# Kernel tuning notes

Hardware: AMD Instinct MI355X
Metric: run time of the kernel (lower is better)

Reference implementation:

```python
import jax, jax.numpy as jnp
import numpy as np

B, H, N, D, S = 32, 4, 8192, 64, 3
EPS = 1e-10


def setup_inputs() -> dict:
    key = jax.random.key(0)
    ks = jax.random.split(key, 9)
    dev = 1.0 / np.sqrt(D + N)  # init scale from initialize_memory()
    memory = jax.random.uniform(ks[0], (B, N, D), minval=-dev, maxval=dev, dtype=jnp.float32)
    k = jax.random.normal(ks[1], (B, H, D), dtype=jnp.float32)
    beta = jax.random.uniform(ks[2], (B, H), dtype=jnp.float32) * 5.0          # key strength >= 0
    pw = jax.nn.softmax(jax.random.normal(ks[3], (B, H, N), dtype=jnp.float32), axis=-1)  # prev weights: simplex
    g = jax.random.uniform(ks[4], (B, H), dtype=jnp.float32)                    # gate in [0,1]
    s = jax.nn.softmax(jax.random.normal(ks[5], (B, H, S), dtype=jnp.float32), axis=-1)   # shift distribution
    gamma = 1.0 + 2.0 * jax.random.uniform(ks[6], (B, H), dtype=jnp.float32)    # sharpening >= 1
    erase = jax.random.uniform(ks[7], (B, H, D), dtype=jnp.float32)             # erase in [0,1]
    add = jax.random.normal(ks[8], (B, H, D), dtype=jnp.float32)
    return {"memory": memory, "k": k, "beta": beta, "pw": pw, "g": g,
            "s": s, "gamma": gamma, "erase": erase, "add": add}


def _ntm_step(memory, k, beta, pw, g, s, gamma, erase, add):
    # --- content addressing: softmax over slots of beta * cosine similarity ---
    kn = k / (jnp.linalg.norm(k, axis=-1, keepdims=True) + EPS)         # [B,H,D]
    mn = memory / (jnp.linalg.norm(memory, axis=-1, keepdims=True) + EPS)  # [B,N,D]
    cos = jnp.einsum('bhd,bnd->bhn', kn, mn)                            # [B,H,N]
    wc = jax.nn.softmax(beta[..., None] * cos, axis=-1)
    # --- location addressing: interpolate, circular shift, sharpen ---
    gb = g[..., None]
    wg = gb * wc + (1.0 - gb) * pw                                      # [B,H,N]
    center = (s.shape[-1] - 1) // 2
    # ws(i) = sum_j wg((i - off_j) mod N) * s(j), off_j = j - center
    ws = sum(s[..., j:j + 1] * jnp.roll(wg, j - center, axis=-1)
             for j in range(s.shape[-1]))
    wgam = ws ** gamma[..., None]
    w = wgam / jnp.sum(wgam, axis=-1, keepdims=True)                    # [B,H,N]
    # --- write: sequential erase/add outer products per head ---
    mem = memory
    for h in range(w.shape[1]):
        e = w[:, h, :, None] * erase[:, h, None, :]                     # [B,N,D]
        a = w[:, h, :, None] * add[:, h, None, :]
        mem = mem * (1.0 - e) + a
    # --- read from updated memory ---
    reading = jnp.einsum('bhn,bnd->bhd', w, mem)                        # [B,H,D]
    return reading


def reference(memory, k, beta, pw, g, s, gamma, erase, add):
    return _ntm_step(memory, k, beta, pw, g, s, gamma, erase, add)
```

## Files before the change

kernel.cpp:

```cpp
#include <hip/hip_runtime.h>
#include <math.h>

#define Bc 32
#define Hc 4
#define Nc 8192
#define Dc 64
#define EPSc 1e-10f

#define T1ROWS 64
#define NT1 (Nc / T1ROWS)
#define T2ROWS 64
#define NT2 (Nc / T2ROWS)
#define T3ROWS 128
#define NT3 (Nc / T3ROWS)

__global__ __launch_bounds__(256) void k_scores(
    const float* __restrict__ mem, const float* __restrict__ kk,
    const float* __restrict__ beta,
    float* __restrict__ tbuf, float* __restrict__ z1p)
{
    const int b = blockIdx.y, tile = blockIdx.x, tid = threadIdx.x;
    const int wave = tid >> 6, lane = tid & 63;

    __shared__ float ks[Hc][Dc];
    __shared__ float wsum[4][Hc];

    {
        float kv = kk[(b * Hc + wave) * Dc + lane];
        float ss = kv * kv;
        #pragma unroll
        for (int off = 32; off; off >>= 1) ss += __shfl_xor(ss, off);
        float scale = beta[b * Hc + wave] / (sqrtf(ss) + EPSc);
        ks[wave][lane] = kv * scale;
    }
    __syncthreads();

    const int r    = tid >> 2;
    const int part = tid & 3;
    const int n    = tile * T1ROWS + r;
    const float4* p4 = reinterpret_cast<const float4*>(
        mem + ((size_t)b * Nc + n) * Dc + part * 16);

    float ss = 0.f;
    float dot[Hc] = {0.f, 0.f, 0.f, 0.f};
    #pragma unroll
    for (int j = 0; j < 4; ++j) {
        float4 v = p4[j];
        ss = fmaf(v.x, v.x, ss); ss = fmaf(v.y, v.y, ss);
        ss = fmaf(v.z, v.z, ss); ss = fmaf(v.w, v.w, ss);
        const int c0 = part * 16 + 4 * j;
        #pragma unroll
        for (int h = 0; h < Hc; ++h) {
            dot[h] = fmaf(v.x, ks[h][c0 + 0], dot[h]);
            dot[h] = fmaf(v.y, ks[h][c0 + 1], dot[h]);
            dot[h] = fmaf(v.z, ks[h][c0 + 2], dot[h]);
            dot[h] = fmaf(v.w, ks[h][c0 + 3], dot[h]);
        }
    }
    #pragma unroll
    for (int off = 1; off <= 2; off <<= 1) {
        ss += __shfl_xor(ss, off);
        #pragma unroll
        for (int h = 0; h < Hc; ++h) dot[h] += __shfl_xor(dot[h], off);
    }
    const float inv = 1.0f / (sqrtf(ss) + EPSc);

    const float tval = expf(dot[part] * inv);
    tbuf[(b * Hc + part) * Nc + n] = tval;

    float v = tval;
    #pragma unroll
    for (int off = 4; off <= 32; off <<= 1) v += __shfl_xor(v, off);
    if (lane < Hc) wsum[wave][lane] = v;
    __syncthreads();
    if (tid < Hc)
        z1p[(b * Hc + tid) * NT1 + tile] =
            wsum[0][tid] + wsum[1][tid] + wsum[2][tid] + wsum[3][tid];
}

__global__ __launch_bounds__(256) void k_shift(
    const float* __restrict__ tbuf, const float* __restrict__ z1p,
    const float* __restrict__ pw, const float* __restrict__ g,
    const float* __restrict__ s, const float* __restrict__ gamma,
    float* __restrict__ wgbuf, float* __restrict__ z2p)
{
    const int b = blockIdx.y, tile = blockIdx.x, tid = threadIdx.x;
    const int h = tid >> 6, lane = tid & 63;

    float v = z1p[(b * Hc + h) * NT1 + lane] + z1p[(b * Hc + h) * NT1 + lane + 64];
    #pragma unroll
    for (int off = 32; off; off >>= 1) v += __shfl_xor(v, off);
    const float iz = 1.0f / v;
    const float invZ1 = __shfl(iz, 0);

    const float gh  = g[b * Hc + h];
    const float gmh = gamma[b * Hc + h];
    const float s0 = s[(b * Hc + h) * 3 + 0];
    const float s1 = s[(b * Hc + h) * 3 + 1];
    const float s2 = s[(b * Hc + h) * 3 + 2];
    const float omg = 1.0f - gh;

    const int n  = tile * T2ROWS + lane;
    const int nm = (n == 0) ? (Nc - 1) : (n - 1);
    const int np = (n == Nc - 1) ? 0 : (n + 1);
    const int base = (b * Hc + h) * Nc;

    const float wg_c = gh * tbuf[base + n]  * invZ1 + omg * pw[base + n];
    const float wg_m = gh * tbuf[base + nm] * invZ1 + omg * pw[base + nm];
    const float wg_p = gh * tbuf[base + np] * invZ1 + omg * pw[base + np];
    const float wsv = s0 * wg_p + s1 * wg_c + s2 * wg_m;
    const float wgam = powf(wsv, gmh);
    wgbuf[base + n] = wgam;

    float pv = wgam;
    #pragma unroll
    for (int off = 32; off; off >>= 1) pv += __shfl_xor(pv, off);
    if (lane == 0) z2p[(b * Hc + h) * NT2 + tile] = pv;
}

__global__ __launch_bounds__(256) void k_update(
    const float* __restrict__ mem, const float* __restrict__ wgbuf,
    const float* __restrict__ z2p, const float* __restrict__ erase,
    const float* __restrict__ add, float* __restrict__ rp)
{
    const int b = blockIdx.y, tile = blockIdx.x, tid = threadIdx.x;
    const int rg = tid >> 6, dl = tid & 63;

    __shared__ float invZ2[Hc];
    {
        float v = z2p[(b * Hc + rg) * NT2 + dl] + z2p[(b * Hc + rg) * NT2 + dl + 64];
        #pragma unroll
        for (int off = 32; off; off >>= 1) v += __shfl_xor(v, off);
        if (dl == 0) invZ2[rg] = 1.0f / v;
    }
    __syncthreads();

    float e[Hc], a[Hc], iz[Hc];
    #pragma unroll
    for (int h = 0; h < Hc; ++h) {
        e[h]  = erase[(b * Hc + h) * Dc + dl];
        a[h]  = add  [(b * Hc + h) * Dc + dl];
        iz[h] = invZ2[h];
    }

    float r[Hc] = {0.f, 0.f, 0.f, 0.f};
    const int n0 = tile * T3ROWS;
    #pragma unroll 4
    for (int i = 0; i < T3ROWS / 4; ++i) {
        const int n = n0 + i * 4 + rg;
        float m = mem[((size_t)b * Nc + n) * Dc + dl];
        float w[Hc];
        #pragma unroll
        for (int h = 0; h < Hc; ++h)
            w[h] = wgbuf[(b * Hc + h) * Nc + n] * iz[h];
        #pragma unroll
        for (int h = 0; h < Hc; ++h)
            m = m * (1.0f - w[h] * e[h]) + w[h] * a[h];
        #pragma unroll
        for (int h = 0; h < Hc; ++h)
            r[h] = fmaf(w[h], m, r[h]);
    }

    __shared__ float acc[4][Hc][Dc];
    #pragma unroll
    for (int h = 0; h < Hc; ++h) acc[rg][h][dl] = r[h];
    __syncthreads();

    const int h = tid >> 6, d = tid & 63;
    const float sum = acc[0][h][d] + acc[1][h][d] + acc[2][h][d] + acc[3][h][d];
    rp[((b * NT3 + tile) * Hc + h) * Dc + d] = sum;
}

__global__ __launch_bounds__(256) void k_final(
    const float* __restrict__ rp, float* __restrict__ out)
{
    const int b = blockIdx.x, tid = threadIdx.x;
    float sum = 0.f;
    #pragma unroll
    for (int t = 0; t < NT3; ++t) sum += rp[(b * NT3 + t) * 256 + tid];
    out[b * 256 + tid] = sum;
}

extern "C" void kernel_launch(void* const* d_in, const int* in_sizes, int n_in,
                              void* d_out, int out_size, void* d_ws, size_t ws_size,
                              hipStream_t stream) {
    const float* mem   = (const float*)d_in[0];
    const float* kk    = (const float*)d_in[1];
    const float* beta  = (const float*)d_in[2];
    const float* pw    = (const float*)d_in[3];
    const float* g     = (const float*)d_in[4];
    const float* s     = (const float*)d_in[5];
    const float* gamma = (const float*)d_in[6];
    const float* erase = (const float*)d_in[7];
    const float* add   = (const float*)d_in[8];
    float* out = (float*)d_out;

    float* ws    = (float*)d_ws;
    float* tbuf  = ws;
    float* wgbuf = tbuf + (size_t)Bc*Hc*Nc;
    float* z1p   = wgbuf + (size_t)Bc*Hc*Nc;
    float* z2p   = z1p + (size_t)Bc*Hc*NT1;
    float* rp    = z2p + (size_t)Bc*Hc*NT2;

    k_scores<<<dim3(NT1, Bc), 256, 0, stream>>>(mem, kk, beta, tbuf, z1p);
    k_shift <<<dim3(NT2, Bc), 256, 0, stream>>>(tbuf, z1p, pw, g, s, gamma, wgbuf, z2p);
    k_update<<<dim3(NT3, Bc), 256, 0, stream>>>(mem, wgbuf, z2p, erase, add, rp);
    k_final <<<Bc, 256, 0, stream>>>(rp, out);
}
```

Before: 50.50 us.

## Vectorize shift and update kernels with float4, fast math, split final reduction

The shift kernel now handles four consecutive slots per thread with float4 loads and stores and uses fast __powf. The update kernel reads memory rows as float4, with 16 threads per row and 16 rows per step, and reduces across 16 row groups in shared memory. Scores use __expf, and the final reduction is spread over 4x more blocks, each reducing a quarter of the tiles across 4 waves. These changes aim to cut memory instruction count and raise parallelism in the small final kernel, at the cost of slightly less accurate exp and pow.

```diff
diff --git a/kernel.cpp b/kernel.cpp
--- a/kernel.cpp
+++ b/kernel.cpp
@@ -9,7 +9,7 @@
 
 #define T1ROWS 64
 #define NT1 (Nc / T1ROWS)
-#define T2ROWS 64
+#define T2ROWS 256
 #define NT2 (Nc / T2ROWS)
 #define T3ROWS 128
 #define NT3 (Nc / T3ROWS)
@@ -65,7 +65,7 @@
     }
     const float inv = 1.0f / (sqrtf(ss) + EPSc);
 
-    const float tval = expf(dot[part] * inv);
+    const float tval = __expf(dot[part] * inv);
     tbuf[(b * Hc + part) * Nc + n] = tval;
 
     float v = tval;
@@ -90,8 +90,7 @@
     float v = z1p[(b * Hc + h) * NT1 + lane] + z1p[(b * Hc + h) * NT1 + lane + 64];
     #pragma unroll
     for (int off = 32; off; off >>= 1) v += __shfl_xor(v, off);
-    const float iz = 1.0f / v;
-    const float invZ1 = __shfl(iz, 0);
+    const float invZ1 = __shfl(1.0f / v, 0);
 
     const float gh  = g[b * Hc + h];
     const float gmh = gamma[b * Hc + h];
@@ -100,19 +99,31 @@
     const float s2 = s[(b * Hc + h) * 3 + 2];
     const float omg = 1.0f - gh;
 
-    const int n  = tile * T2ROWS + lane;
-    const int nm = (n == 0) ? (Nc - 1) : (n - 1);
-    const int np = (n == Nc - 1) ? 0 : (n + 1);
+    const int n0   = tile * T2ROWS + lane * 4;
     const int base = (b * Hc + h) * Nc;
-
-    const float wg_c = gh * tbuf[base + n]  * invZ1 + omg * pw[base + n];
-    const float wg_m = gh * tbuf[base + nm] * invZ1 + omg * pw[base + nm];
-    const float wg_p = gh * tbuf[base + np] * invZ1 + omg * pw[base + np];
-    const float wsv = s0 * wg_p + s1 * wg_c + s2 * wg_m;
-    const float wgam = powf(wsv, gmh);
-    wgbuf[base + n] = wgam;
-
-    float pv = wgam;
+    const int nm = (n0 == 0) ? (Nc - 1) : (n0 - 1);
+    const int np = (n0 + 4 == Nc) ? 0 : (n0 + 4);
+
+    const float4 t4  = *reinterpret_cast<const float4*>(tbuf + base + n0);
+    const float4 p4  = *reinterpret_cast<const float4*>(pw   + base + n0);
+    const float  tm = tbuf[base + nm], pm = pw[base + nm];
+    const float  tp = tbuf[base + np], pp = pw[base + np];
+
+    const float wgm1 = gh * tm   * invZ1 + omg * pm;
+    const float wg0  = gh * t4.x * invZ1 + omg * p4.x;
+    const float wg1  = gh * t4.y * invZ1 + omg * p4.y;
+    const float wg2  = gh * t4.z * invZ1 + omg * p4.z;
+    const float wg3  = gh * t4.w * invZ1 + omg * p4.w;
+    const float wg4  = gh * tp   * invZ1 + omg * pp;
+
+    float4 wgam;
+    wgam.x = __powf(s0 * wg1 + s1 * wg0 + s2 * wgm1, gmh);
+    wgam.y = __powf(s0 * wg2 + s1 * wg1 + s2 * wg0,  gmh);
+    wgam.z = __powf(s0 * wg3 + s1 * wg2 + s2 * wg1,  gmh);
+    wgam.w = __powf(s0 * wg4 + s1 * wg3 + s2 * wg2,  gmh);
+    *reinterpret_cast<float4*>(wgbuf + base + n0) = wgam;
+
+    float pv = wgam.x + wgam.y + wgam.z + wgam.w;
     #pragma unroll
     for (int off = 32; off; off >>= 1) pv += __shfl_xor(pv, off);
     if (lane == 0) z2p[(b * Hc + h) * NT2 + tile] = pv;
@@ -124,61 +135,88 @@
     const float* __restrict__ add, float* __restrict__ rp)
 {
     const int b = blockIdx.y, tile = blockIdx.x, tid = threadIdx.x;
-    const int rg = tid >> 6, dl = tid & 63;
+    const int part = tid & 15;
+    const int rw   = tid >> 4;
 
     __shared__ float invZ2[Hc];
     {
-        float v = z2p[(b * Hc + rg) * NT2 + dl] + z2p[(b * Hc + rg) * NT2 + dl + 64];
+        const int wave = tid >> 6, lane = tid & 63;
+        float v = (lane < NT2) ? z2p[(b * Hc + wave) * NT2 + lane] : 0.f;
         #pragma unroll
         for (int off = 32; off; off >>= 1) v += __shfl_xor(v, off);
-        if (dl == 0) invZ2[rg] = 1.0f / v;
-    }
-    __syncthreads();
-
-    float e[Hc], a[Hc], iz[Hc];
+        if (lane == 0) invZ2[wave] = 1.0f / v;
+    }
+    __syncthreads();
+
+    float4 e4[Hc], a4[Hc];
+    float iz[Hc];
     #pragma unroll
     for (int h = 0; h < Hc; ++h) {
-        e[h]  = erase[(b * Hc + h) * Dc + dl];
-        a[h]  = add  [(b * Hc + h) * Dc + dl];
+        e4[h] = *reinterpret_cast<const float4*>(erase + (b * Hc + h) * Dc + part * 4);
+        a4[h] = *reinterpret_cast<const float4*>(add   + (b * Hc + h) * Dc + part * 4);
         iz[h] = invZ2[h];
     }
 
-    float r[Hc] = {0.f, 0.f, 0.f, 0.f};
+    float4 r4[Hc];
+    #pragma unroll
+    for (int h = 0; h < Hc; ++h) r4[h] = make_float4(0.f, 0.f, 0.f, 0.f);
+
     const int n0 = tile * T3ROWS;
     #pragma unroll 4
-    for (int i = 0; i < T3ROWS / 4; ++i) {
-        const int n = n0 + i * 4 + rg;
-        float m = mem[((size_t)b * Nc + n) * Dc + dl];
+    for (int i = 0; i < T3ROWS / 16; ++i) {
+        const int n = n0 + i * 16 + rw;
+        float4 m4 = *reinterpret_cast<const float4*>(
+            mem + ((size_t)b * Nc + n) * Dc + part * 4);
         float w[Hc];
         #pragma unroll
         for (int h = 0; h < Hc; ++h)
             w[h] = wgbuf[(b * Hc + h) * Nc + n] * iz[h];
         #pragma unroll
-        for (int h = 0; h < Hc; ++h)
-            m = m * (1.0f - w[h] * e[h]) + w[h] * a[h];
-        #pragma unroll
-        for (int h = 0; h < Hc; ++h)
-            r[h] = fmaf(w[h], m, r[h]);
-    }
-
-    __shared__ float acc[4][Hc][Dc];
-    #pragma unroll
-    for (int h = 0; h < Hc; ++h) acc[rg][h][dl] = r[h];
+        for (int h = 0; h < Hc; ++h) {
+            m4.x = m4.x * (1.0f - w[h] * e4[h].x) + w[h] * a4[h].x;
+            m4.y = m4.y * (1.0f - w[h] * e4[h].y) + w[h] * a4[h].y;
+            m4.z = m4.z * (1.0f - w[h] * e4[h].z) + w[h] * a4[h].z;
+            m4.w = m4.w * (1.0f - w[h] * e4[h].w) + w[h] * a4[h].w;
+        }
+        #pragma unroll
+        for (int h = 0; h < Hc; ++h) {
+            r4[h].x = fmaf(w[h], m4.x, r4[h].x);
+            r4[h].y = fmaf(w[h], m4.y, r4[h].y);
+            r4[h].z = fmaf(w[h], m4.z, r4[h].z);
+            r4[h].w = fmaf(w[h], m4.w, r4[h].w);
+        }
+    }
+
+    __shared__ float4 acc[16][Hc][16];
+    #pragma unroll
+    for (int h = 0; h < Hc; ++h) acc[rw][h][part] = r4[h];
     __syncthreads();
 
     const int h = tid >> 6, d = tid & 63;
-    const float sum = acc[0][h][d] + acc[1][h][d] + acc[2][h][d] + acc[3][h][d];
+    float sum = 0.f;
+    #pragma unroll
+    for (int r2 = 0; r2 < 16; ++r2)
+        sum += reinterpret_cast<const float*>(&acc[r2][h][d >> 2])[d & 3];
     rp[((b * NT3 + tile) * Hc + h) * Dc + d] = sum;
 }
 
 __global__ __launch_bounds__(256) void k_final(
     const float* __restrict__ rp, float* __restrict__ out)
 {
-    const int b = blockIdx.x, tid = threadIdx.x;
+    const int b = blockIdx.x, q = blockIdx.y, tid = threadIdx.x;
+    const int o = tid & 63, tg = tid >> 6;
+
     float sum = 0.f;
     #pragma unroll
-    for (int t = 0; t < NT3; ++t) sum += rp[(b * NT3 + t) * 256 + tid];
-    out[b * 256 + tid] = sum;
+    for (int t = 0; t < NT3 / 4; ++t)
+        sum += rp[(b * NT3 + tg * (NT3 / 4) + t) * 256 + q * 64 + o];
+
+    __shared__ float acc[4][64];
+    acc[tg][o] = sum;
+    __syncthreads();
+    if (tid < 64)
+        out[b * 256 + q * 64 + tid] =
+            acc[0][tid] + acc[1][tid] + acc[2][tid] + acc[3][tid];
 }
 
 extern "C" void kernel_launch(void* const* d_in, const int* in_sizes, int n_in,
@@ -205,5 +243,5 @@
     k_scores<<<dim3(NT1, Bc), 256, 0, stream>>>(mem, kk, beta, tbuf, z1p);
     k_shift <<<dim3(NT2, Bc), 256, 0, stream>>>(tbuf, z1p, pw, g, s, gamma, wgbuf, z2p);
     k_update<<<dim3(NT3, Bc), 256, 0, stream>>>(mem, wgbuf, z2p, erase, add, rp);
-    k_final <<<Bc, 256, 0, stream>>>(rp, out);
-}
+    k_final <<<dim3(Bc, 4), 256, 0, stream>>>(rp, out);
+}
```

Result: faster. 42.65 us (-15.6%).
